# Performance work log

Hardware: AMD Instinct MI355X
Metric: run time of the kernel (lower is better)

The kernel has to match this reference:

```python
import jax, jax.numpy as jnp
import numpy as np

EMBED_DIM = 1024
NUM_HEADS = 16
HEAD_DIM = EMBED_DIM // NUM_HEADS
SCALING = HEAD_DIM ** -0.5


def setup_inputs() -> dict:
    key = jax.random.key(0)
    k1, k2, k3, k4, k5 = jax.random.split(key, 5)
    B, S, E, H = 2, 2048, EMBED_DIM, NUM_HEADS
    x = jax.random.normal(k1, (B, S, E), dtype=jnp.float32)
    # nn.Linear weights: [out_features, in_features]
    W_A = jax.random.normal(k2, (H, E), dtype=jnp.float32) * (E ** -0.5)
    W_V = jax.random.normal(k3, (E, E), dtype=jnp.float32) * (E ** -0.5)
    W_O = jax.random.normal(k4, (E, E), dtype=jnp.float32) * (E ** -0.5)
    b_O = jax.random.normal(k5, (E,), dtype=jnp.float32) * 0.01
    return {"x": x, "W_A": W_A, "W_V": W_V, "W_O": W_O, "b_O": b_O}


def reference(x, W_A, W_V, W_O, b_O):
    B, S, E = x.shape
    H, D = NUM_HEADS, HEAD_DIM
    # per-head scalar attention logits, softmax over sequence dim
    z = jnp.einsum('bse,he->bsh', x, W_A) * SCALING          # [B,S,H]
    z = jax.nn.softmax(z, axis=1)                            # softmax over seq
    zp = jnp.transpose(z, (0, 2, 1))                         # [B,H,S]
    # causal roll matrix: roll[b,h,i,j] = z[b,h,i-j] for j<=i else 0
    i = jnp.arange(S)[:, None]
    j = jnp.arange(S)[None, :]
    idx = (i - j) % S                                        # [S,S]
    tril = (j <= i).astype(x.dtype)                          # causal mask
    roll = zp[:, :, idx] * tril                              # [B,H,S,S]
    # values split into heads
    v = jnp.einsum('bse,fe->bsf', x, W_V).reshape(B, S, H, D)  # [B,S,H,D]
    out = jnp.einsum('bhij,bjhd->bihd', roll, v).reshape(B, S, E)
    return jnp.einsum('bse,fe->bsf', out, W_O) + b_O
```

## Files before the change

kernel.cpp:

```cpp
#include <hip/hip_runtime.h>
#include <hip/hip_bf16.h>
#include <stdint.h>

typedef unsigned short u16;
typedef short short8 __attribute__((ext_vector_type(8)));
typedef float f32x4 __attribute__((ext_vector_type(4)));

#define SEQ 2048
#define EMB 1024
#define NH 16
#define HD 64
#define ZP 2112

__device__ inline u16 f2bf(float f) {
    uint32_t u = __builtin_bit_cast(uint32_t, f);
    uint32_t r = (u + 0x7FFFu + ((u >> 16) & 1u)) >> 16;
    return (u16)r;
}

__device__ inline void gload16(const void* g, void* l) {
    __builtin_amdgcn_global_load_lds(
        (const __attribute__((address_space(1))) void*)g,
        (__attribute__((address_space(3))) void*)l, 16, 0, 0);
}

__global__ __launch_bounds__(256) void cast_all(const float* __restrict__ x,
                                                const float* __restrict__ W_V,
                                                const float* __restrict__ W_O,
                                                u16* __restrict__ xb,
                                                u16* __restrict__ wvb,
                                                u16* __restrict__ wob) {
    int bid = blockIdx.x, t = threadIdx.x;
    const float* src;
    u16* dst;
    int j;
    if (bid < 4096) { j = bid * 256 + t; src = x; dst = xb; }
    else {
        j = (bid - 4096) * 256 + t;
        if (j < 262144) { src = W_V; dst = wvb; }
        else { j -= 262144; src = W_O; dst = wob; }
    }
    float4 f = reinterpret_cast<const float4*>(src)[j];
    union { u16 u[4]; uint2 v; } o;
    o.u[0] = f2bf(f.x); o.u[1] = f2bf(f.y); o.u[2] = f2bf(f.z); o.u[3] = f2bf(f.w);
    reinterpret_cast<uint2*>(dst)[j] = o.v;
}

__global__ __launch_bounds__(256) void logits_kernel(const float* __restrict__ x,
                                                     const float* __restrict__ W_A,
                                                     float* __restrict__ zl) {
    __shared__ float wa[NH * EMB];
    int t = threadIdx.x;
    for (int i = t; i < NH * EMB / 4; i += 256)
        reinterpret_cast<float4*>(wa)[i] = reinterpret_cast<const float4*>(W_A)[i];
    __syncthreads();
    int w = t >> 6, l = t & 63;
    int row0 = blockIdx.x * 16 + w * 4;
    for (int rr = 0; rr < 4; rr++) {
        int gs = row0 + rr;
        int b = gs >> 11, s = gs & 2047;
        const float* xr = x + (size_t)gs * EMB;
        float xv[16];
#pragma unroll
        for (int q = 0; q < 16; q++) xv[q] = xr[l + 64 * q];
#pragma unroll
        for (int h = 0; h < NH; h++) {
            float a = 0.f;
#pragma unroll
            for (int q = 0; q < 16; q++) a += xv[q] * wa[h * EMB + l + 64 * q];
#pragma unroll
            for (int off = 32; off; off >>= 1) a += __shfl_xor(a, off);
            if (l == h) zl[((size_t)b * NH + h) * SEQ + s] = a * 0.125f;
        }
    }
}

__device__ void softmax_body(const float* __restrict__ zl, u16* __restrict__ zr, int bh) {
    const float* src = zl + (size_t)bh * SEQ;
    int t = threadIdx.x;
    int w = t >> 6, l = t & 63;
    __shared__ float red[4];
    __shared__ float bc;
    float v[8];
#pragma unroll
    for (int q = 0; q < 8; q++) v[q] = src[t + 256 * q];
    float m = v[0];
#pragma unroll
    for (int q = 1; q < 8; q++) m = fmaxf(m, v[q]);
#pragma unroll
    for (int off = 32; off; off >>= 1) m = fmaxf(m, __shfl_xor(m, off));
    if (l == 0) red[w] = m;
    __syncthreads();
    if (t == 0) bc = fmaxf(fmaxf(red[0], red[1]), fmaxf(red[2], red[3]));
    __syncthreads();
    m = bc;
    float s = 0.f;
#pragma unroll
    for (int q = 0; q < 8; q++) { v[q] = expf(v[q] - m); s += v[q]; }
#pragma unroll
    for (int off = 32; off; off >>= 1) s += __shfl_xor(s, off);
    if (l == 0) red[w] = s;
    __syncthreads();
    if (t == 0) bc = red[0] + red[1] + red[2] + red[3];
    __syncthreads();
    float inv = 1.0f / bc;
#pragma unroll
    for (int q = 0; q < 8; q++) {
        int sidx = t + 256 * q;
        zr[(size_t)bh * ZP + (SEQ - 1 - sidx)] = f2bf(v[q] * inv);
    }
    if (t < ZP - SEQ) zr[(size_t)bh * ZP + SEQ + t] = 0;
}

template <int OUTMODE, int MAP, bool SM>
__global__ __launch_bounds__(256) void gemm64(const u16* __restrict__ A,
                                              const u16* __restrict__ Bw,
                                              u16* __restrict__ Cb, float* __restrict__ Cf,
                                              const float* __restrict__ bias,
                                              int M, int N, int K,
                                              const float* __restrict__ zl,
                                              u16* __restrict__ zr) {
    if constexpr (SM) {
        if (blockIdx.x >= 512) { softmax_body(zl, zr, blockIdx.x - 512); return; }
    }
    __shared__ u16 As[2][128 * 64];
    __shared__ u16 Bs[2][64 * 64];
    const int t = threadIdx.x;
    const int i = blockIdx.x;
    int xg, yg;
    if constexpr (MAP == 0) { xg = (i & 7) * 8 + ((i >> 3) & 7); yg = i >> 6; }
    else                    { yg = (i & 7) * 4 + ((i >> 3) & 3); xg = i >> 5; }
    const int m0 = yg * 128, n0 = xg * 64;
    const int w = t >> 6, l = t & 63;
    const int wr = w >> 1, wc = w & 1;
    const int lrow = l & 15, lk = l >> 4;
    const int r7 = lrow & 7;

    const int srow = t >> 3;
    const int scb = ((t & 7) ^ ((t >> 3) & 7)) * 8;
    const u16* gA = A + (size_t)(m0 + srow) * K + scb;
    const u16* gB = Bw + (size_t)(n0 + srow) * K + scb;
    const int ldst = w * 512;

    f32x4 acc[4][2];
#pragma unroll
    for (int a = 0; a < 4; a++)
#pragma unroll
        for (int b = 0; b < 2; b++) acc[a][b] = (f32x4){0.f, 0.f, 0.f, 0.f};

    const int NT = K >> 6;
    const size_t rk32 = (size_t)32 * K;
#pragma unroll
    for (int c = 0; c < 4; c++) gload16(gA + c * rk32, &As[0][ldst + 2048 * c]);
#pragma unroll
    for (int c = 0; c < 2; c++) gload16(gB + c * rk32, &Bs[0][ldst + 2048 * c]);
    __syncthreads();

    for (int kt = 0; kt < NT; kt++) {
        const int cur = kt & 1;
        if (kt + 1 < NT) {
            const int k0 = (kt + 1) * 64;
#pragma unroll
            for (int c = 0; c < 4; c++) gload16(gA + k0 + c * rk32, &As[cur ^ 1][ldst + 2048 * c]);
#pragma unroll
            for (int c = 0; c < 2; c++) gload16(gB + k0 + c * rk32, &Bs[cur ^ 1][ldst + 2048 * c]);
        }
#pragma unroll
        for (int kk = 0; kk < 2; kk++) {
            const int cs = ((kk * 4 + lk) ^ r7) * 8;
            short8 af[4], bf2[2];
#pragma unroll
            for (int mi = 0; mi < 4; mi++)
                af[mi] = *reinterpret_cast<const short8*>(
                    &As[cur][(wr * 64 + mi * 16 + lrow) * 64 + cs]);
#pragma unroll
            for (int ni = 0; ni < 2; ni++)
                bf2[ni] = *reinterpret_cast<const short8*>(
                    &Bs[cur][(wc * 32 + ni * 16 + lrow) * 64 + cs]);
#pragma unroll
            for (int mi = 0; mi < 4; mi++)
#pragma unroll
                for (int ni = 0; ni < 2; ni++)
                    acc[mi][ni] = __builtin_amdgcn_mfma_f32_16x16x32_bf16(af[mi], bf2[ni], acc[mi][ni], 0, 0, 0);
        }
        __syncthreads();
    }
#pragma unroll
    for (int mi = 0; mi < 4; mi++)
#pragma unroll
        for (int ni = 0; ni < 2; ni++)
#pragma unroll
            for (int r = 0; r < 4; r++) {
                int row = m0 + wr * 64 + mi * 16 + lk * 4 + r;
                int col = n0 + wc * 32 + ni * 16 + lrow;
                if constexpr (OUTMODE == 0)
                    Cb[(size_t)row * N + col] = f2bf(acc[mi][ni][r]);
                else
                    Cf[(size_t)row * N + col] = acc[mi][ni][r] + bias[col];
            }
}

__global__ __launch_bounds__(256) void conv_kernel(const u16* __restrict__ zr,
                                                   const u16* __restrict__ vt2,
                                                   u16* __restrict__ cv) {
    const int i = blockIdx.x;
    const int bh = (i & 7) * 4 + ((i >> 3) & 3);
    const int rest = i >> 5;
    const int b = bh >> 4, h = bh & 15;
    __shared__ uint zsl[2176];
    const int t = threadIdx.x;
    {
        const uint* zp = reinterpret_cast<const uint*>(zr + (size_t)bh * ZP);
        for (int q = t; q < 1088; q += 256) {
            uint v0 = (q < 1056) ? zp[q] : 0u;
            uint v1 = (q < 1055) ? zp[q + 1] : 0u;
            zsl[q] = v0;
            zsl[1088 + q] = (v0 >> 16) | (v1 << 16);
        }
    }
    __syncthreads();

    const int w = t >> 6, l = t & 63;
    const int task = rest * 4 + w;
    const int pp = task >> 1;
    const int ch = task & 1;
    const int lrow = l & 15;
    const int lk8 = (l >> 4) * 8;
    const int col0 = ch * 32;
    const int ebase = h * 64 + col0;
    const size_t boff = (size_t)b * SEQ;

    union U { uint d[4]; short8 s8; };

    int slices[2] = {pp, 63 - pp};
#pragma unroll 1
    for (int si = 0; si < 2; si++) {
        const int s = slices[si];
        const int row0 = s * 32;
        const int nk = s + 1;
        f32x4 acc[2][2];
#pragma unroll
        for (int a = 0; a < 2; a++)
#pragma unroll
            for (int c = 0; c < 2; c++) acc[a][c] = (f32x4){0.f, 0.f, 0.f, 0.f};

        const int obase = 2047 - row0 - lrow + lk8;

        auto loadB = [&](int k0, U* bf) {
#pragma unroll
            for (int ni = 0; ni < 2; ni++) {
                const u16* p = vt2 + (((size_t)(ebase + ni * 16 + lrow)) << 12) + boff + k0 + lk8;
                *reinterpret_cast<uint4*>(bf[ni].d) = *reinterpret_cast<const uint4*>(p);
            }
        };
        auto loadA = [&](int k0, U* af) {
#pragma unroll
            for (int mi = 0; mi < 2; mi++) {
                int o = obase - mi * 16 + k0;
                uint adw = (uint)(o >> 1) + (uint)((o & 1) * 1088);
#pragma unroll
                for (int q = 0; q < 4; q++) af[mi].d[q] = zsl[adw + q];
            }
        };

        U a0[2], a1[2], b0[2], b1[2];
        loadB(0, b0);
        loadB(32, b1);
        loadA(0, a0);
        int k = 0;
        for (; k + 1 < nk; k += 2) {
            loadA((k + 1) * 32, a1);
#pragma unroll
            for (int mi = 0; mi < 2; mi++)
#pragma unroll
                for (int ni = 0; ni < 2; ni++)
                    acc[mi][ni] = __builtin_amdgcn_mfma_f32_16x16x32_bf16(a0[mi].s8, b0[ni].s8, acc[mi][ni], 0, 0, 0);
            if (k + 2 < nk) loadB((k + 2) * 32, b0);
            loadA((k + 2) * 32, a0);
#pragma unroll
            for (int mi = 0; mi < 2; mi++)
#pragma unroll
                for (int ni = 0; ni < 2; ni++)
                    acc[mi][ni] = __builtin_amdgcn_mfma_f32_16x16x32_bf16(a1[mi].s8, b1[ni].s8, acc[mi][ni], 0, 0, 0);
            if (k + 3 < nk) loadB((k + 3) * 32, b1);
        }
        if (nk & 1) {
#pragma unroll
            for (int mi = 0; mi < 2; mi++)
#pragma unroll
                for (int ni = 0; ni < 2; ni++)
                    acc[mi][ni] = __builtin_amdgcn_mfma_f32_16x16x32_bf16(a0[mi].s8, b0[ni].s8, acc[mi][ni], 0, 0, 0);
        }
#pragma unroll
        for (int mi = 0; mi < 2; mi++)
#pragma unroll
            for (int ni = 0; ni < 2; ni++)
#pragma unroll
                for (int r = 0; r < 4; r++) {
                    int row = row0 + mi * 16 + (l >> 4) * 4 + r;
                    int col = col0 + ni * 16 + lrow;
                    cv[((size_t)b * SEQ + row) * EMB + h * 64 + col] = f2bf(acc[mi][ni][r]);
                }
    }
}

extern "C" void kernel_launch(void* const* d_in, const int* in_sizes, int n_in,
                              void* d_out, int out_size, void* d_ws, size_t ws_size,
                              hipStream_t stream) {
    const float* x   = (const float*)d_in[0];
    const float* W_A = (const float*)d_in[1];
    const float* W_V = (const float*)d_in[2];
    const float* W_O = (const float*)d_in[3];
    const float* b_O = (const float*)d_in[4];

    char* ws = (char*)d_ws;
    u16*   xb  = (u16*)(ws + 0);
    u16*   wvb = (u16*)(ws + 8388608);
    u16*   wob = (u16*)(ws + 10485760);
    float* zl  = (float*)(ws + 12582912);
    u16*   zr  = (u16*)(ws + 12845056);
    u16*   vt2 = (u16*)(ws + 12980224);
    u16*   cv  = (u16*)(ws + 21368832);

    cast_all<<<6144, 256, 0, stream>>>(x, W_V, W_O, xb, wvb, wob);
    logits_kernel<<<256, 256, 0, stream>>>(x, W_A, zl);
    gemm64<0, 0, true><<<544, 256, 0, stream>>>(wvb, xb, vt2, nullptr, nullptr,
                                                1024, 4096, 1024, zl, zr);
    conv_kernel<<<512, 256, 0, stream>>>(zr, vt2, cv);
    gemm64<1, 1, false><<<512, 256, 0, stream>>>(cv, wob, nullptr, (float*)d_out, b_O,
                                                 4096, 1024, 1024, nullptr, nullptr);
}
```

Baseline: 103.1 us.

## Enlarge GEMM tiles to 128x128 with 512-thread blocks and XCD-aware block mapping

Both projection GEMMs move from 128x64 tiles with 256 threads to 128x128 tiles with 512 threads (8 waves), which halves the grid and raises operand reuse per block. Block indices are remapped so consecutive blocks scatter across the 8 XCDs, and the per-iteration __syncthreads is replaced by explicit vmcnt waits plus raw s_barrier to overlap the next tile's global-to-LDS loads. The fused softmax path is adapted to 512 threads. The cost is more LDS per block and fewer blocks (256 on 256 CUs), which leaves one wave of blocks and lower occupancy per CU.

```diff
diff --git a/kernel.cpp b/kernel.cpp
--- a/kernel.cpp
+++ b/kernel.cpp
@@ -75,72 +75,83 @@
     }
 }
 
-__device__ void softmax_body(const float* __restrict__ zl, u16* __restrict__ zr, int bh) {
+__device__ void softmax_body512(const float* __restrict__ zl, u16* __restrict__ zr, int bh) {
     const float* src = zl + (size_t)bh * SEQ;
     int t = threadIdx.x;
     int w = t >> 6, l = t & 63;
-    __shared__ float red[4];
+    __shared__ float red[8];
     __shared__ float bc;
-    float v[8];
-#pragma unroll
-    for (int q = 0; q < 8; q++) v[q] = src[t + 256 * q];
-    float m = v[0];
-#pragma unroll
-    for (int q = 1; q < 8; q++) m = fmaxf(m, v[q]);
+    float v[4];
+#pragma unroll
+    for (int q = 0; q < 4; q++) v[q] = src[t + 512 * q];
+    float m = fmaxf(fmaxf(v[0], v[1]), fmaxf(v[2], v[3]));
 #pragma unroll
     for (int off = 32; off; off >>= 1) m = fmaxf(m, __shfl_xor(m, off));
     if (l == 0) red[w] = m;
     __syncthreads();
-    if (t == 0) bc = fmaxf(fmaxf(red[0], red[1]), fmaxf(red[2], red[3]));
+    if (t == 0) {
+        float mm = red[0];
+#pragma unroll
+        for (int q = 1; q < 8; q++) mm = fmaxf(mm, red[q]);
+        bc = mm;
+    }
     __syncthreads();
     m = bc;
     float s = 0.f;
 #pragma unroll
-    for (int q = 0; q < 8; q++) { v[q] = expf(v[q] - m); s += v[q]; }
+    for (int q = 0; q < 4; q++) { v[q] = expf(v[q] - m); s += v[q]; }
 #pragma unroll
     for (int off = 32; off; off >>= 1) s += __shfl_xor(s, off);
     if (l == 0) red[w] = s;
     __syncthreads();
-    if (t == 0) bc = red[0] + red[1] + red[2] + red[3];
+    if (t == 0) {
+        float ss = 0.f;
+#pragma unroll
+        for (int q = 0; q < 8; q++) ss += red[q];
+        bc = ss;
+    }
     __syncthreads();
     float inv = 1.0f / bc;
 #pragma unroll
-    for (int q = 0; q < 8; q++) {
-        int sidx = t + 256 * q;
+    for (int q = 0; q < 4; q++) {
+        int sidx = t + 512 * q;
         zr[(size_t)bh * ZP + (SEQ - 1 - sidx)] = f2bf(v[q] * inv);
     }
     if (t < ZP - SEQ) zr[(size_t)bh * ZP + SEQ + t] = 0;
 }
 
 template <int OUTMODE, int MAP, bool SM>
-__global__ __launch_bounds__(256) void gemm64(const u16* __restrict__ A,
-                                              const u16* __restrict__ Bw,
-                                              u16* __restrict__ Cb, float* __restrict__ Cf,
-                                              const float* __restrict__ bias,
-                                              int M, int N, int K,
-                                              const float* __restrict__ zl,
-                                              u16* __restrict__ zr) {
+__global__ __launch_bounds__(512) void gemm128(const u16* __restrict__ A,
+                                               const u16* __restrict__ Bw,
+                                               u16* __restrict__ Cb, float* __restrict__ Cf,
+                                               const float* __restrict__ bias,
+                                               int M, int N, int K,
+                                               const float* __restrict__ zl,
+                                               u16* __restrict__ zr) {
     if constexpr (SM) {
-        if (blockIdx.x >= 512) { softmax_body(zl, zr, blockIdx.x - 512); return; }
+        if (blockIdx.x >= 256) { softmax_body512(zl, zr, blockIdx.x - 256); return; }
     }
     __shared__ u16 As[2][128 * 64];
-    __shared__ u16 Bs[2][64 * 64];
+    __shared__ u16 Bs[2][128 * 64];
     const int t = threadIdx.x;
     const int i = blockIdx.x;
+    const int wg = (i & 7) * 32 + (i >> 3);
     int xg, yg;
-    if constexpr (MAP == 0) { xg = (i & 7) * 8 + ((i >> 3) & 7); yg = i >> 6; }
-    else                    { yg = (i & 7) * 4 + ((i >> 3) & 3); xg = i >> 5; }
-    const int m0 = yg * 128, n0 = xg * 64;
+    if constexpr (MAP == 0) { xg = wg >> 3; yg = wg & 7; }
+    else                    { yg = wg >> 3; xg = wg & 7; }
+    const int m0 = yg * 128, n0 = xg * 128;
     const int w = t >> 6, l = t & 63;
-    const int wr = w >> 1, wc = w & 1;
+    const int wr = w >> 2, wc = w & 3;
     const int lrow = l & 15, lk = l >> 4;
     const int r7 = lrow & 7;
 
-    const int srow = t >> 3;
-    const int scb = ((t & 7) ^ ((t >> 3) & 7)) * 8;
-    const u16* gA = A + (size_t)(m0 + srow) * K + scb;
-    const u16* gB = Bw + (size_t)(n0 + srow) * K + scb;
-    const int ldst = w * 512;
+    const int srow = w * 16 + (l >> 3);
+    const int scb = ((l & 7) ^ (l >> 3)) * 8;
+    const u16* gA0 = A + (size_t)(m0 + srow) * K + scb;
+    const u16* gA1 = gA0 + (size_t)8 * K;
+    const u16* gB0 = Bw + (size_t)(n0 + srow) * K + scb;
+    const u16* gB1 = gB0 + (size_t)8 * K;
+    const int ldsbase = w * 16 * 64;
 
     f32x4 acc[4][2];
 #pragma unroll
@@ -149,22 +160,25 @@
         for (int b = 0; b < 2; b++) acc[a][b] = (f32x4){0.f, 0.f, 0.f, 0.f};
 
     const int NT = K >> 6;
-    const size_t rk32 = (size_t)32 * K;
-#pragma unroll
-    for (int c = 0; c < 4; c++) gload16(gA + c * rk32, &As[0][ldst + 2048 * c]);
-#pragma unroll
-    for (int c = 0; c < 2; c++) gload16(gB + c * rk32, &Bs[0][ldst + 2048 * c]);
-    __syncthreads();
+    gload16(gA0, &As[0][ldsbase]);
+    gload16(gA1, &As[0][ldsbase + 512]);
+    gload16(gB0, &Bs[0][ldsbase]);
+    gload16(gB1, &Bs[0][ldsbase + 512]);
 
     for (int kt = 0; kt < NT; kt++) {
         const int cur = kt & 1;
         if (kt + 1 < NT) {
             const int k0 = (kt + 1) * 64;
-#pragma unroll
-            for (int c = 0; c < 4; c++) gload16(gA + k0 + c * rk32, &As[cur ^ 1][ldst + 2048 * c]);
-#pragma unroll
-            for (int c = 0; c < 2; c++) gload16(gB + k0 + c * rk32, &Bs[cur ^ 1][ldst + 2048 * c]);
-        }
+            gload16(gA0 + k0, &As[cur ^ 1][ldsbase]);
+            gload16(gA1 + k0, &As[cur ^ 1][ldsbase + 512]);
+            gload16(gB0 + k0, &Bs[cur ^ 1][ldsbase]);
+            gload16(gB1 + k0, &Bs[cur ^ 1][ldsbase + 512]);
+            asm volatile("s_waitcnt vmcnt(4)" ::: "memory");
+        } else {
+            asm volatile("s_waitcnt vmcnt(0)" ::: "memory");
+        }
+        __builtin_amdgcn_sched_barrier(0);
+        __builtin_amdgcn_s_barrier();
 #pragma unroll
         for (int kk = 0; kk < 2; kk++) {
             const int cs = ((kk * 4 + lk) ^ r7) * 8;
@@ -183,7 +197,7 @@
                 for (int ni = 0; ni < 2; ni++)
                     acc[mi][ni] = __builtin_amdgcn_mfma_f32_16x16x32_bf16(af[mi], bf2[ni], acc[mi][ni], 0, 0, 0);
         }
-        __syncthreads();
+        __builtin_amdgcn_s_barrier();
     }
 #pragma unroll
     for (int mi = 0; mi < 4; mi++)
@@ -324,9 +338,9 @@
 
     cast_all<<<6144, 256, 0, stream>>>(x, W_V, W_O, xb, wvb, wob);
     logits_kernel<<<256, 256, 0, stream>>>(x, W_A, zl);
-    gemm64<0, 0, true><<<544, 256, 0, stream>>>(wvb, xb, vt2, nullptr, nullptr,
-                                                1024, 4096, 1024, zl, zr);
+    gemm128<0, 0, true><<<288, 512, 0, stream>>>(wvb, xb, vt2, nullptr, nullptr,
+                                                 1024, 4096, 1024, zl, zr);
     conv_kernel<<<512, 256, 0, stream>>>(zr, vt2, cv);
-    gemm64<1, 1, false><<<512, 256, 0, stream>>>(cv, wob, nullptr, (float*)d_out, b_O,
-                                                 4096, 1024, 1024, nullptr, nullptr);
-}
+    gemm128<1, 1, false><<<256, 512, 0, stream>>>(cv, wob, nullptr, (float*)d_out, b_O,
+                                                  4096, 1024, 1024, nullptr, nullptr);
+}
```

Measured after the change: 104.7 us. Within noise of the previous version (+1.5%).

## Replace 128x64 GEMM with 64x64 tiles using intra-block split-K across waves

Applied to the files above, without the earlier changes.

The two projection GEMMs now use 64x64 output tiles. Each of the four waves computes the full tile over its own quarter of K, and the partial sums are reduced through LDS before a vectorized store. This doubles the block count, raises the occupancy hint to 4 blocks per SM, and reuses the LDS staging buffer for the reduction. In exchange it drops the double-buffered prefetch (each step loads, then syncs, then computes) and adds a serialized multi-step LDS reduction at the end.

```diff
diff --git a/kernel.cpp b/kernel.cpp
--- a/kernel.cpp
+++ b/kernel.cpp
@@ -79,7 +79,7 @@
     const float* src = zl + (size_t)bh * SEQ;
     int t = threadIdx.x;
     int w = t >> 6, l = t & 63;
-    __shared__ float red[4];
+    __shared__ float red4[4];
     __shared__ float bc;
     float v[8];
 #pragma unroll
@@ -89,9 +89,9 @@
     for (int q = 1; q < 8; q++) m = fmaxf(m, v[q]);
 #pragma unroll
     for (int off = 32; off; off >>= 1) m = fmaxf(m, __shfl_xor(m, off));
-    if (l == 0) red[w] = m;
-    __syncthreads();
-    if (t == 0) bc = fmaxf(fmaxf(red[0], red[1]), fmaxf(red[2], red[3]));
+    if (l == 0) red4[w] = m;
+    __syncthreads();
+    if (t == 0) bc = fmaxf(fmaxf(red4[0], red4[1]), fmaxf(red4[2], red4[3]));
     __syncthreads();
     m = bc;
     float s = 0.f;
@@ -99,9 +99,9 @@
     for (int q = 0; q < 8; q++) { v[q] = expf(v[q] - m); s += v[q]; }
 #pragma unroll
     for (int off = 32; off; off >>= 1) s += __shfl_xor(s, off);
-    if (l == 0) red[w] = s;
-    __syncthreads();
-    if (t == 0) bc = red[0] + red[1] + red[2] + red[3];
+    if (l == 0) red4[w] = s;
+    __syncthreads();
+    if (t == 0) bc = red4[0] + red4[1] + red4[2] + red4[3];
     __syncthreads();
     float inv = 1.0f / bc;
 #pragma unroll
@@ -113,91 +113,126 @@
 }
 
 template <int OUTMODE, int MAP, bool SM>
-__global__ __launch_bounds__(256) void gemm64(const u16* __restrict__ A,
-                                              const u16* __restrict__ Bw,
-                                              u16* __restrict__ Cb, float* __restrict__ Cf,
-                                              const float* __restrict__ bias,
-                                              int M, int N, int K,
-                                              const float* __restrict__ zl,
-                                              u16* __restrict__ zr) {
+__global__ __launch_bounds__(256, 4) void gemm_ks(const u16* __restrict__ A,
+                                                  const u16* __restrict__ Bw,
+                                                  u16* __restrict__ Cb, float* __restrict__ Cf,
+                                                  const float* __restrict__ bias,
+                                                  int M, int N, int K,
+                                                  const float* __restrict__ zl,
+                                                  u16* __restrict__ zr) {
+    const int nblk = (M >> 6) * (N >> 6);
     if constexpr (SM) {
-        if (blockIdx.x >= 512) { softmax_body(zl, zr, blockIdx.x - 512); return; }
-    }
-    __shared__ u16 As[2][128 * 64];
-    __shared__ u16 Bs[2][64 * 64];
+        if ((int)blockIdx.x >= nblk) { softmax_body(zl, zr, blockIdx.x - nblk); return; }
+    }
+    __shared__ float red[2][64][68];
+    u16* As = (u16*)&red[0][0][0];
+    u16* Bs = As + 8192;
+
     const int t = threadIdx.x;
     const int i = blockIdx.x;
+    const int cpx = nblk >> 3;
+    const int wg = (i & 7) * cpx + (i >> 3);
     int xg, yg;
-    if constexpr (MAP == 0) { xg = (i & 7) * 8 + ((i >> 3) & 7); yg = i >> 6; }
-    else                    { yg = (i & 7) * 4 + ((i >> 3) & 3); xg = i >> 5; }
-    const int m0 = yg * 128, n0 = xg * 64;
+    if constexpr (MAP == 0) { xg = wg >> 4; yg = wg & 15; }
+    else                    { yg = wg >> 4; xg = wg & 15; }
+    const int m0 = yg * 64, n0 = xg * 64;
     const int w = t >> 6, l = t & 63;
-    const int wr = w >> 1, wc = w & 1;
     const int lrow = l & 15, lk = l >> 4;
-    const int r7 = lrow & 7;
-
-    const int srow = t >> 3;
-    const int scb = ((t & 7) ^ ((t >> 3) & 7)) * 8;
-    const u16* gA = A + (size_t)(m0 + srow) * K + scb;
-    const u16* gB = Bw + (size_t)(n0 + srow) * K + scb;
-    const int ldst = w * 512;
-
-    f32x4 acc[4][2];
+    const int Kq = K >> 2;
+
+    const u16* sA[4];
+    const u16* sB[4];
+    int db[4];
+#pragma unroll
+    for (int q = 0; q < 4; q++) {
+        int row = w * 16 + q * 4 + (l >> 4);
+        int cp = l & 15;
+        int C = cp ^ (row & 15);
+        int kb = (C >> 2) * Kq + (C & 3) * 8;
+        sA[q] = A + (size_t)(m0 + row) * K + kb;
+        sB[q] = Bw + (size_t)(n0 + row) * K + kb;
+        db[q] = (w * 16 + q * 4) * 128;
+    }
+    int ro[4];
+#pragma unroll
+    for (int mi = 0; mi < 4; mi++)
+        ro[mi] = (mi * 16 + lrow) * 128 + (((w * 4 + lk) ^ lrow) * 8);
+
+    f32x4 acc[4][4];
 #pragma unroll
     for (int a = 0; a < 4; a++)
 #pragma unroll
-        for (int b = 0; b < 2; b++) acc[a][b] = (f32x4){0.f, 0.f, 0.f, 0.f};
-
-    const int NT = K >> 6;
-    const size_t rk32 = (size_t)32 * K;
-#pragma unroll
-    for (int c = 0; c < 4; c++) gload16(gA + c * rk32, &As[0][ldst + 2048 * c]);
-#pragma unroll
-    for (int c = 0; c < 2; c++) gload16(gB + c * rk32, &Bs[0][ldst + 2048 * c]);
-    __syncthreads();
-
-    for (int kt = 0; kt < NT; kt++) {
-        const int cur = kt & 1;
-        if (kt + 1 < NT) {
-            const int k0 = (kt + 1) * 64;
-#pragma unroll
-            for (int c = 0; c < 4; c++) gload16(gA + k0 + c * rk32, &As[cur ^ 1][ldst + 2048 * c]);
-#pragma unroll
-            for (int c = 0; c < 2; c++) gload16(gB + k0 + c * rk32, &Bs[cur ^ 1][ldst + 2048 * c]);
-        }
-#pragma unroll
-        for (int kk = 0; kk < 2; kk++) {
-            const int cs = ((kk * 4 + lk) ^ r7) * 8;
-            short8 af[4], bf2[2];
-#pragma unroll
-            for (int mi = 0; mi < 4; mi++)
-                af[mi] = *reinterpret_cast<const short8*>(
-                    &As[cur][(wr * 64 + mi * 16 + lrow) * 64 + cs]);
-#pragma unroll
-            for (int ni = 0; ni < 2; ni++)
-                bf2[ni] = *reinterpret_cast<const short8*>(
-                    &Bs[cur][(wc * 32 + ni * 16 + lrow) * 64 + cs]);
-#pragma unroll
-            for (int mi = 0; mi < 4; mi++)
-#pragma unroll
-                for (int ni = 0; ni < 2; ni++)
-                    acc[mi][ni] = __builtin_amdgcn_mfma_f32_16x16x32_bf16(af[mi], bf2[ni], acc[mi][ni], 0, 0, 0);
-        }
+        for (int b = 0; b < 4; b++) acc[a][b] = (f32x4){0.f, 0.f, 0.f, 0.f};
+
+    const int NS = Kq >> 5;
+    for (int s = 0; s < NS; s++) {
+        const int ko = s * 32;
+#pragma unroll
+        for (int q = 0; q < 4; q++) gload16(sA[q] + ko, As + db[q]);
+#pragma unroll
+        for (int q = 0; q < 4; q++) gload16(sB[q] + ko, Bs + db[q]);
         __syncthreads();
-    }
-#pragma unroll
-    for (int mi = 0; mi < 4; mi++)
-#pragma unroll
-        for (int ni = 0; ni < 2; ni++)
-#pragma unroll
-            for (int r = 0; r < 4; r++) {
-                int row = m0 + wr * 64 + mi * 16 + lk * 4 + r;
-                int col = n0 + wc * 32 + ni * 16 + lrow;
-                if constexpr (OUTMODE == 0)
-                    Cb[(size_t)row * N + col] = f2bf(acc[mi][ni][r]);
-                else
-                    Cf[(size_t)row * N + col] = acc[mi][ni][r] + bias[col];
-            }
+        short8 af[4], bf[4];
+#pragma unroll
+        for (int mi = 0; mi < 4; mi++)
+            af[mi] = *reinterpret_cast<const short8*>(&As[ro[mi]]);
+#pragma unroll
+        for (int ni = 0; ni < 4; ni++)
+            bf[ni] = *reinterpret_cast<const short8*>(&Bs[ro[ni]]);
+#pragma unroll
+        for (int mi = 0; mi < 4; mi++)
+#pragma unroll
+            for (int ni = 0; ni < 4; ni++)
+                acc[mi][ni] = __builtin_amdgcn_mfma_f32_16x16x32_bf16(af[mi], bf[ni], acc[mi][ni], 0, 0, 0);
+        __syncthreads();
+    }
+
+    auto dump = [&](int slot) {
+#pragma unroll
+        for (int mi = 0; mi < 4; mi++)
+#pragma unroll
+            for (int ni = 0; ni < 4; ni++)
+#pragma unroll
+                for (int rr = 0; rr < 4; rr++)
+                    red[slot][mi * 16 + lk * 4 + rr][ni * 16 + lrow] = acc[mi][ni][rr];
+    };
+    auto addin = [&](int slot) {
+#pragma unroll
+        for (int mi = 0; mi < 4; mi++)
+#pragma unroll
+            for (int ni = 0; ni < 4; ni++)
+#pragma unroll
+                for (int rr = 0; rr < 4; rr++)
+                    acc[mi][ni][rr] += red[slot][mi * 16 + lk * 4 + rr][ni * 16 + lrow];
+    };
+    if (w == 1) dump(0);
+    if (w == 3) dump(1);
+    __syncthreads();
+    if (w == 0) addin(0);
+    if (w == 2) addin(1);
+    __syncthreads();
+    if (w == 2) dump(0);
+    __syncthreads();
+    if (w == 0) { addin(0); dump(0); }
+    __syncthreads();
+
+    const int sr = t >> 2, sc = (t & 3) * 16;
+    if constexpr (OUTMODE == 0) {
+        union { u16 u[16]; uint4 v[2]; } o;
+#pragma unroll
+        for (int j = 0; j < 16; j++) o.u[j] = f2bf(red[0][sr][sc + j]);
+        uint4* p = reinterpret_cast<uint4*>(Cb + (size_t)(m0 + sr) * N + n0 + sc);
+        p[0] = o.v[0];
+        p[1] = o.v[1];
+    } else {
+        float o[16];
+#pragma unroll
+        for (int j = 0; j < 16; j++) o[j] = red[0][sr][sc + j] + bias[n0 + sc + j];
+        float4* p = reinterpret_cast<float4*>(Cf + (size_t)(m0 + sr) * N + n0 + sc);
+#pragma unroll
+        for (int j4 = 0; j4 < 4; j4++)
+            p[j4] = (float4){o[j4 * 4], o[j4 * 4 + 1], o[j4 * 4 + 2], o[j4 * 4 + 3]};
+    }
 }
 
 __global__ __launch_bounds__(256) void conv_kernel(const u16* __restrict__ zr,
@@ -296,10 +331,10 @@
 #pragma unroll
             for (int ni = 0; ni < 2; ni++)
 #pragma unroll
-                for (int r = 0; r < 4; r++) {
-                    int row = row0 + mi * 16 + (l >> 4) * 4 + r;
+                for (int rr = 0; rr < 4; rr++) {
+                    int row = row0 + mi * 16 + (l >> 4) * 4 + rr;
                     int col = col0 + ni * 16 + lrow;
-                    cv[((size_t)b * SEQ + row) * EMB + h * 64 + col] = f2bf(acc[mi][ni][r]);
+                    cv[((size_t)b * SEQ + row) * EMB + h * 64 + col] = f2bf(acc[mi][ni][rr]);
                 }
     }
 }
@@ -324,9 +359,9 @@
 
     cast_all<<<6144, 256, 0, stream>>>(x, W_V, W_O, xb, wvb, wob);
     logits_kernel<<<256, 256, 0, stream>>>(x, W_A, zl);
-    gemm64<0, 0, true><<<544, 256, 0, stream>>>(wvb, xb, vt2, nullptr, nullptr,
-                                                1024, 4096, 1024, zl, zr);
+    gemm_ks<0, 0, true><<<1056, 256, 0, stream>>>(wvb, xb, vt2, nullptr, nullptr,
+                                                  1024, 4096, 1024, zl, zr);
     conv_kernel<<<512, 256, 0, stream>>>(zr, vt2, cv);
-    gemm64<1, 1, false><<<512, 256, 0, stream>>>(cv, wob, nullptr, (float*)d_out, b_O,
-                                                 4096, 1024, 1024, nullptr, nullptr);
-}
+    gemm_ks<1, 1, false><<<1024, 256, 0, stream>>>(cv, wob, nullptr, (float*)d_out, b_O,
+                                                   4096, 1024, 1024, nullptr, nullptr);
+}
```

New measurement: 118.0 us. 14.4% more time.

## Fuse x cast into logits kernel and stage V tiles in LDS for causal conv

Applied to the files above, without the earlier changes.

The x-to-bf16 cast moves into the logits kernel, which already reads each x row, and the weight casts share the same launch. This removes one kernel launch and a second full read of x. The causal roll-conv kernel is restructured so that each block covers a 256-row group with four waves sharing double-buffered, XOR-swizzled V tiles in LDS, loaded via global_load_lds. This replaces per-wave direct global loads and cuts the block count in half. The trade-off is extra block-wide barriers per K step, plus idle waves on tail steps where k0 exceeds a wave's causal limit.

```diff
diff --git a/kernel.cpp b/kernel.cpp
--- a/kernel.cpp
+++ b/kernel.cpp
@@ -24,38 +24,33 @@
         (__attribute__((address_space(3))) void*)l, 16, 0, 0);
 }
 
-__global__ __launch_bounds__(256) void cast_all(const float* __restrict__ x,
-                                                const float* __restrict__ W_V,
-                                                const float* __restrict__ W_O,
-                                                u16* __restrict__ xb,
-                                                u16* __restrict__ wvb,
-                                                u16* __restrict__ wob) {
-    int bid = blockIdx.x, t = threadIdx.x;
-    const float* src;
-    u16* dst;
-    int j;
-    if (bid < 4096) { j = bid * 256 + t; src = x; dst = xb; }
-    else {
-        j = (bid - 4096) * 256 + t;
+__global__ __launch_bounds__(256) void cast_logits(const float* __restrict__ x,
+                                                   const float* __restrict__ W_A,
+                                                   const float* __restrict__ W_V,
+                                                   const float* __restrict__ W_O,
+                                                   u16* __restrict__ xb,
+                                                   u16* __restrict__ wvb,
+                                                   u16* __restrict__ wob,
+                                                   float* __restrict__ zl) {
+    const int bid = blockIdx.x, t = threadIdx.x;
+    if (bid >= 256) {
+        int j = (bid - 256) * 256 + t;
+        const float* src;
+        u16* dst;
         if (j < 262144) { src = W_V; dst = wvb; }
         else { j -= 262144; src = W_O; dst = wob; }
-    }
-    float4 f = reinterpret_cast<const float4*>(src)[j];
-    union { u16 u[4]; uint2 v; } o;
-    o.u[0] = f2bf(f.x); o.u[1] = f2bf(f.y); o.u[2] = f2bf(f.z); o.u[3] = f2bf(f.w);
-    reinterpret_cast<uint2*>(dst)[j] = o.v;
-}
-
-__global__ __launch_bounds__(256) void logits_kernel(const float* __restrict__ x,
-                                                     const float* __restrict__ W_A,
-                                                     float* __restrict__ zl) {
+        float4 f = reinterpret_cast<const float4*>(src)[j];
+        union { u16 u[4]; uint2 v; } o;
+        o.u[0] = f2bf(f.x); o.u[1] = f2bf(f.y); o.u[2] = f2bf(f.z); o.u[3] = f2bf(f.w);
+        reinterpret_cast<uint2*>(dst)[j] = o.v;
+        return;
+    }
     __shared__ float wa[NH * EMB];
-    int t = threadIdx.x;
     for (int i = t; i < NH * EMB / 4; i += 256)
         reinterpret_cast<float4*>(wa)[i] = reinterpret_cast<const float4*>(W_A)[i];
     __syncthreads();
-    int w = t >> 6, l = t & 63;
-    int row0 = blockIdx.x * 16 + w * 4;
+    const int w = t >> 6, l = t & 63;
+    const int row0 = bid * 16 + w * 4;
     for (int rr = 0; rr < 4; rr++) {
         int gs = row0 + rr;
         int b = gs >> 11, s = gs & 2047;
@@ -63,6 +58,9 @@
         float xv[16];
 #pragma unroll
         for (int q = 0; q < 16; q++) xv[q] = xr[l + 64 * q];
+        u16* xw = xb + (size_t)gs * EMB;
+#pragma unroll
+        for (int q = 0; q < 16; q++) xw[l + 64 * q] = f2bf(xv[q]);
 #pragma unroll
         for (int h = 0; h < NH; h++) {
             float a = 0.f;
@@ -79,7 +77,7 @@
     const float* src = zl + (size_t)bh * SEQ;
     int t = threadIdx.x;
     int w = t >> 6, l = t & 63;
-    __shared__ float red[4];
+    __shared__ float red4[4];
     __shared__ float bc;
     float v[8];
 #pragma unroll
@@ -89,9 +87,9 @@
     for (int q = 1; q < 8; q++) m = fmaxf(m, v[q]);
 #pragma unroll
     for (int off = 32; off; off >>= 1) m = fmaxf(m, __shfl_xor(m, off));
-    if (l == 0) red[w] = m;
-    __syncthreads();
-    if (t == 0) bc = fmaxf(fmaxf(red[0], red[1]), fmaxf(red[2], red[3]));
+    if (l == 0) red4[w] = m;
+    __syncthreads();
+    if (t == 0) bc = fmaxf(fmaxf(red4[0], red4[1]), fmaxf(red4[2], red4[3]));
     __syncthreads();
     m = bc;
     float s = 0.f;
@@ -99,9 +97,9 @@
     for (int q = 0; q < 8; q++) { v[q] = expf(v[q] - m); s += v[q]; }
 #pragma unroll
     for (int off = 32; off; off >>= 1) s += __shfl_xor(s, off);
-    if (l == 0) red[w] = s;
-    __syncthreads();
-    if (t == 0) bc = red[0] + red[1] + red[2] + red[3];
+    if (l == 0) red4[w] = s;
+    __syncthreads();
+    if (t == 0) bc = red4[0] + red4[1] + red4[2] + red4[3];
     __syncthreads();
     float inv = 1.0f / bc;
 #pragma unroll
@@ -200,14 +198,17 @@
             }
 }
 
-__global__ __launch_bounds__(256) void conv_kernel(const u16* __restrict__ zr,
-                                                   const u16* __restrict__ vt2,
-                                                   u16* __restrict__ cv) {
+__global__ __launch_bounds__(256) void conv2(const u16* __restrict__ zr,
+                                             const u16* __restrict__ vt2,
+                                             u16* __restrict__ cv) {
     const int i = blockIdx.x;
     const int bh = (i & 7) * 4 + ((i >> 3) & 3);
     const int rest = i >> 5;
+    const int ch = rest & 1;
+    const int gsel = rest >> 1;
     const int b = bh >> 4, h = bh & 15;
     __shared__ uint zsl[2176];
+    __shared__ u16 Bt[2][32 * 64];
     const int t = threadIdx.x;
     {
         const uint* zp = reinterpret_cast<const uint*>(zr + (size_t)bh * ZP);
@@ -218,88 +219,75 @@
             zsl[1088 + q] = (v0 >> 16) | (v1 << 16);
         }
     }
-    __syncthreads();
-
     const int w = t >> 6, l = t & 63;
-    const int task = rest * 4 + w;
-    const int pp = task >> 1;
-    const int ch = task & 1;
-    const int lrow = l & 15;
-    const int lk8 = (l >> 4) * 8;
-    const int col0 = ch * 32;
-    const int ebase = h * 64 + col0;
+    const int lrow = l & 15, lk = l >> 4, lk8 = lk * 8;
+    const int ebase = h * 64 + ch * 32;
     const size_t boff = (size_t)b * SEQ;
 
+    const int rB = w * 8 + (l >> 3);
+    const int Csrc = (l & 7) ^ (rB & 7);
+    const u16* gB = vt2 + (((size_t)(ebase + rB)) << 12) + boff + Csrc * 8;
+    const int dbase = w * 512;
+    __syncthreads();
+
     union U { uint d[4]; short8 s8; };
-
-    int slices[2] = {pp, 63 - pp};
+    const int gms[2] = {gsel, 7 - gsel};
 #pragma unroll 1
     for (int si = 0; si < 2; si++) {
-        const int s = slices[si];
-        const int row0 = s * 32;
-        const int nk = s + 1;
-        f32x4 acc[2][2];
-#pragma unroll
-        for (int a = 0; a < 2; a++)
+        const int gm = gms[si];
+        const int kend = (gm + 1) * 256;
+        const int ns = kend >> 6;
+        const int r0 = gm * 256 + w * 64;
+        const int wkmax = r0 + 64;
+        const int obase0 = 2047 - r0 - lrow + lk8;
+        f32x4 acc[4][2];
+#pragma unroll
+        for (int a = 0; a < 4; a++)
 #pragma unroll
             for (int c = 0; c < 2; c++) acc[a][c] = (f32x4){0.f, 0.f, 0.f, 0.f};
 
-        const int obase = 2047 - row0 - lrow + lk8;
-
-        auto loadB = [&](int k0, U* bf) {
-#pragma unroll
-            for (int ni = 0; ni < 2; ni++) {
-                const u16* p = vt2 + (((size_t)(ebase + ni * 16 + lrow)) << 12) + boff + k0 + lk8;
-                *reinterpret_cast<uint4*>(bf[ni].d) = *reinterpret_cast<const uint4*>(p);
+        gload16(gB, &Bt[0][dbase]);
+        for (int s = 0; s < ns; s++) {
+            const int cur = s & 1;
+            const int k0 = s * 64;
+            if (s + 1 < ns) gload16(gB + k0 + 64, &Bt[cur ^ 1][dbase]);
+            __syncthreads();
+            if (k0 < wkmax) {
+#pragma unroll
+                for (int kk = 0; kk < 2; kk++) {
+                    U af[4];
+                    short8 bf2[2];
+#pragma unroll
+                    for (int mi = 0; mi < 4; mi++) {
+                        int o = obase0 - mi * 16 + k0 + kk * 32;
+                        uint adw = (uint)(o >> 1) + (uint)((o & 1) * 1088);
+#pragma unroll
+                        for (int q = 0; q < 4; q++) af[mi].d[q] = zsl[adw + q];
+                    }
+#pragma unroll
+                    for (int ni = 0; ni < 2; ni++) {
+                        int row = ni * 16 + lrow;
+                        int c2 = (((kk * 4 + lk) ^ (row & 7))) * 8;
+                        bf2[ni] = *reinterpret_cast<const short8*>(&Bt[cur][row * 64 + c2]);
+                    }
+#pragma unroll
+                    for (int mi = 0; mi < 4; mi++)
+#pragma unroll
+                        for (int ni = 0; ni < 2; ni++)
+                            acc[mi][ni] = __builtin_amdgcn_mfma_f32_16x16x32_bf16(af[mi].s8, bf2[ni], acc[mi][ni], 0, 0, 0);
+                }
             }
-        };
-        auto loadA = [&](int k0, U* af) {
-#pragma unroll
-            for (int mi = 0; mi < 2; mi++) {
-                int o = obase - mi * 16 + k0;
-                uint adw = (uint)(o >> 1) + (uint)((o & 1) * 1088);
-#pragma unroll
-                for (int q = 0; q < 4; q++) af[mi].d[q] = zsl[adw + q];
-            }
-        };
-
-        U a0[2], a1[2], b0[2], b1[2];
-        loadB(0, b0);
-        loadB(32, b1);
-        loadA(0, a0);
-        int k = 0;
-        for (; k + 1 < nk; k += 2) {
-            loadA((k + 1) * 32, a1);
-#pragma unroll
-            for (int mi = 0; mi < 2; mi++)
-#pragma unroll
-                for (int ni = 0; ni < 2; ni++)
-                    acc[mi][ni] = __builtin_amdgcn_mfma_f32_16x16x32_bf16(a0[mi].s8, b0[ni].s8, acc[mi][ni], 0, 0, 0);
-            if (k + 2 < nk) loadB((k + 2) * 32, b0);
-            loadA((k + 2) * 32, a0);
-#pragma unroll
-            for (int mi = 0; mi < 2; mi++)
-#pragma unroll
-                for (int ni = 0; ni < 2; ni++)
-                    acc[mi][ni] = __builtin_amdgcn_mfma_f32_16x16x32_bf16(a1[mi].s8, b1[ni].s8, acc[mi][ni], 0, 0, 0);
-            if (k + 3 < nk) loadB((k + 3) * 32, b1);
-        }
-        if (nk & 1) {
-#pragma unroll
-            for (int mi = 0; mi < 2; mi++)
-#pragma unroll
-                for (int ni = 0; ni < 2; ni++)
-                    acc[mi][ni] = __builtin_amdgcn_mfma_f32_16x16x32_bf16(a0[mi].s8, b0[ni].s8, acc[mi][ni], 0, 0, 0);
-        }
-#pragma unroll
-        for (int mi = 0; mi < 2; mi++)
+            __syncthreads();
+        }
+#pragma unroll
+        for (int mi = 0; mi < 4; mi++)
 #pragma unroll
             for (int ni = 0; ni < 2; ni++)
 #pragma unroll
-                for (int r = 0; r < 4; r++) {
-                    int row = row0 + mi * 16 + (l >> 4) * 4 + r;
-                    int col = col0 + ni * 16 + lrow;
-                    cv[((size_t)b * SEQ + row) * EMB + h * 64 + col] = f2bf(acc[mi][ni][r]);
+                for (int rr = 0; rr < 4; rr++) {
+                    int row = r0 + mi * 16 + lk * 4 + rr;
+                    int col = ebase + ni * 16 + lrow;
+                    cv[((size_t)b * SEQ + row) * EMB + col] = f2bf(acc[mi][ni][rr]);
                 }
     }
 }
@@ -322,11 +310,10 @@
     u16*   vt2 = (u16*)(ws + 12980224);
     u16*   cv  = (u16*)(ws + 21368832);
 
-    cast_all<<<6144, 256, 0, stream>>>(x, W_V, W_O, xb, wvb, wob);
-    logits_kernel<<<256, 256, 0, stream>>>(x, W_A, zl);
+    cast_logits<<<2304, 256, 0, stream>>>(x, W_A, W_V, W_O, xb, wvb, wob, zl);
     gemm64<0, 0, true><<<544, 256, 0, stream>>>(wvb, xb, vt2, nullptr, nullptr,
                                                 1024, 4096, 1024, zl, zr);
-    conv_kernel<<<512, 256, 0, stream>>>(zr, vt2, cv);
+    conv2<<<256, 256, 0, stream>>>(zr, vt2, cv);
     gemm64<1, 1, false><<<512, 256, 0, stream>>>(cv, wob, nullptr, (float*)d_out, b_O,
                                                  4096, 1024, 1024, nullptr, nullptr);
 }
```

Measured after the change: 99.89 us. -3.1%, faster.
